# Kernel optimization log

Measured on AMD Instinct MI355X. Metric: run time of the kernel, lower is better.

## Reference

```python
import jax, jax.numpy as jnp
import numpy as np

V_IPC, N_ROLES, D = 50000, 16, 256
B, L = 2048, 64
F_BIB, H1, H2, D_OUT = 512, 1024, 1024, 512
N_EXP, N_CLS = 8, 10
LN_EPS = 1e-5


def setup_inputs() -> dict:
    key = jax.random.key(0)
    ks = jax.random.split(key, 24)
    s = 0.05
    ipc_emb = jax.random.normal(ks[0], (V_IPC, D), jnp.float32) * s
    ipc_emb = ipc_emb.at[0].set(0.0)  # padding_idx=0
    role_emb = jax.random.normal(ks[1], (N_ROLES, D), jnp.float32) * s
    role_emb = role_emb.at[0].set(0.0)
    inp = {
        "ipc_indices": jax.random.randint(ks[2], (B, L), 0, V_IPC),
        "role_indices": jax.random.randint(ks[3], (B, L), 0, N_ROLES),
        "bibliometric_features": jax.random.normal(ks[4], (B, F_BIB), jnp.float32),
        "ipc_padding_mask": jax.random.randint(ks[5], (B, L), 0, 2).astype(jnp.int32),
        "top_k": 2,
        "ipc_emb": ipc_emb,
        "role_emb": role_emb,
        "Wq": jax.random.normal(ks[6], (D, D), jnp.float32) * s,
        "bq": jnp.zeros((D,), jnp.float32),
        "Wk": jax.random.normal(ks[7], (D, D), jnp.float32) * s,
        "bk": jnp.zeros((D,), jnp.float32),
        "Wv": jax.random.normal(ks[8], (D, D), jnp.float32) * s,
        "bv": jnp.zeros((D,), jnp.float32),
        "global_context": jax.random.normal(ks[9], (D,), jnp.float32) * s,
        "ln_g": jnp.ones((D,), jnp.float32),
        "ln_b": jnp.zeros((D,), jnp.float32),
        "gate_W": jax.random.normal(ks[10], (D, N_EXP), jnp.float32) * s,
        "gate_b": jnp.zeros((N_EXP,), jnp.float32),
        "expert_biases": jnp.zeros((N_EXP,), jnp.float32),
        "W1": jax.random.normal(ks[11], (N_EXP, F_BIB, H1), jnp.float32) * s,
        "b1": jnp.zeros((N_EXP, H1), jnp.float32),
        "W2": jax.random.normal(ks[12], (N_EXP, H1, H2), jnp.float32) * s,
        "b2": jnp.zeros((N_EXP, H2), jnp.float32),
        "W3": jax.random.normal(ks[13], (N_EXP, H2, D_OUT), jnp.float32) * s,
        "b3": jnp.zeros((N_EXP, D_OUT), jnp.float32),
        "head_W": jax.random.normal(ks[14], (D_OUT, N_CLS), jnp.float32) * s,
        "head_b": jnp.zeros((N_CLS,), jnp.float32),
    }
    return inp


def reference(ipc_indices, role_indices, bibliometric_features, ipc_padding_mask, top_k,
              ipc_emb, role_emb, Wq, bq, Wk, bk, Wv, bv, global_context, ln_g, ln_b,
              gate_W, gate_b, expert_biases, W1, b1, W2, b2, W3, b3, head_W, head_b):
    # embeddings + role combine  -> [B, L, D]
    x = ipc_emb[ipc_indices] + role_emb[role_indices]
    # attention pooling with a global learned query (same query for every batch row)
    keys = x @ Wk + bk                                  # [B, L, D]
    values = x @ Wv + bv                                # [B, L, D]
    q = global_context @ Wq + bq                        # [D]
    scores = jnp.einsum('d,bld->bl', q, keys)           # [B, L]
    scores = jnp.where(ipc_padding_mask == 0, -1e9, scores)
    attn = jax.nn.softmax(scores, axis=-1)              # [B, L]
    pooled = jnp.einsum('bl,bld->bd', attn, values)     # [B, D]
    mu = pooled.mean(-1, keepdims=True)
    var = ((pooled - mu) ** 2).mean(-1, keepdims=True)
    router_in = (pooled - mu) / jnp.sqrt(var + LN_EPS) * ln_g + ln_b
    # router: select with biased scores, gate with unbiased scores
    affinity = router_in @ gate_W + gate_b              # [B, E]
    sel_scores = affinity + expert_biases
    _, idx = jax.lax.top_k(sel_scores, top_k)           # [B, K]
    gw = jax.nn.softmax(jnp.take_along_axis(affinity, idx, axis=-1), axis=-1)  # [B, K]
    # dense all-expert MLP (reference form of masked per-expert loop)
    h = jax.nn.relu(jnp.einsum('bi,eih->ebh', bibliometric_features, W1) + b1[:, None, :])
    h = jax.nn.relu(jnp.einsum('ebh,ehj->ebj', h, W2) + b2[:, None, :])
    eo = jnp.einsum('ebj,ejo->ebo', h, W3) + b3[:, None, :]  # [E, B, O]
    # gather each token's top-k expert outputs and combine
    bidx = jnp.arange(idx.shape[0])[:, None]            # [B, 1]
    sel_out = eo[idx, bidx]                             # [B, K, O]
    moe_out = jnp.einsum('bk,bko->bo', gw, sel_out)     # [B, O]
    logits = moe_out @ head_W + head_b                  # [B, n_classes]
    return logits, idx
```

## Files before the change

kernel.cpp:

```cpp
#include <hip/hip_runtime.h>
#include <hip/hip_bf16.h>
#include <math.h>


#define LN_EPS 1e-5f

typedef __bf16 bf16_t;
typedef __bf16 bf16x8 __attribute__((ext_vector_type(8)));
typedef float f32x4 __attribute__((ext_vector_type(4)));

struct f4x2 { float4 a, b; };
__device__ __forceinline__ f4x2 ldA8(const float* p) {
  f4x2 v; v.a = *(const float4*)p; v.b = *(const float4*)(p + 4); return v;
}
__device__ __forceinline__ bf16x8 cvt8(const f4x2& v) {
  bf16x8 o;
  o[0] = (bf16_t)v.a.x; o[1] = (bf16_t)v.a.y; o[2] = (bf16_t)v.a.z; o[3] = (bf16_t)v.a.w;
  o[4] = (bf16_t)v.b.x; o[5] = (bf16_t)v.b.y; o[6] = (bf16_t)v.b.z; o[7] = (bf16_t)v.b.w;
  return o;
}

__global__ __launch_bounds__(256)
void transpose_prep(const float* __restrict__ W1, const float* __restrict__ W2,
                    const float* __restrict__ W3, bf16_t* __restrict__ B1,
                    bf16_t* __restrict__ B2, bf16_t* __restrict__ B3,
                    const float* __restrict__ Wq, const float* __restrict__ bq,
                    const float* __restrict__ Wk, const float* __restrict__ bk,
                    const float* __restrict__ gc, float* __restrict__ kq_out) {
  __shared__ float tile[64][65];
  const int z = blockIdx.z;
  if (z == 24) {
    if (blockIdx.y >= 2) return;
    float* q = &tile[0][0];
    float* red = &tile[0][0] + 256;
    const int t = threadIdx.x, bi = blockIdx.y * 16 + blockIdx.x;
    float s = bq[t];
    for (int d = 0; d < 256; d++) s += gc[d] * Wq[d * 256 + t];
    q[t] = s;
    __syncthreads();
    const int rl = t >> 5, sl = t & 31;
    const int r = bi * 8 + rl;
    float p = 0.f;
#pragma unroll
    for (int i = 0; i < 8; i++) { const int d = sl + 32 * i; p += Wk[r * 256 + d] * q[d]; }
#pragma unroll
    for (int o = 16; o > 0; o >>= 1) p += __shfl_down(p, o, 32);
    if (sl == 0) kq_out[r] = p;
    if (bi == 0) {
      float z2 = q[t] * bk[t];
      const int lane = t & 63, wave = t >> 6;
#pragma unroll
      for (int o = 32; o > 0; o >>= 1) z2 += __shfl_down(z2, o);
      if (lane == 0) red[wave] = z2;
      __syncthreads();
      if (t == 0) kq_out[256] = red[0] + red[1] + red[2] + red[3];
    }
    return;
  }
  const float* W; bf16_t* Bft; int K, N, e;
  if (z < 8)       { W = W1; Bft = B1; K = 512;  N = 1024; e = z; }
  else if (z < 16) { W = W2; Bft = B2; K = 1024; N = 1024; e = z - 8; }
  else             { W = W3; Bft = B3; K = 1024; N = 512;  e = z - 16; }
  const int n0 = blockIdx.x * 64, k0 = blockIdx.y * 64;
  if (n0 >= N || k0 >= K) return;
  const float* Wp = W + (size_t)e * K * N;
  bf16_t* Bp = Bft + (size_t)e * N * K;
  const int tq = threadIdx.x & 15, th = threadIdx.x >> 4;
#pragma unroll
  for (int i = 0; i < 4; i++) {
    const int row = th + 16 * i;
    *(float4*)&tile[row][tq * 4] = *(const float4*)(Wp + (size_t)(k0 + row) * N + n0 + tq * 4);
  }
  __syncthreads();
  const int lane = threadIdx.x & 63, sub = threadIdx.x >> 6;
  const int nk = K >> 5;
#pragma unroll
  for (int it = 0; it < 2; it++) {
    const int fid = sub + it * 4;
    const int ntl = fid & 3, ktl = fid >> 2;
    const int n_l = ntl * 16 + (lane & 15);
    const int k_l = ktl * 32 + (lane >> 4) * 8;
    bf16x8 o;
#pragma unroll
    for (int j = 0; j < 8; j++) o[j] = (bf16_t)tile[k_l + j][n_l];
    const size_t idx = ((((size_t)(n0 >> 4) + ntl) * nk + (k0 >> 5) + ktl) * 64 + lane) * 8;
    *(bf16x8*)(Bp + idx) = o;
  }
}

__global__ __launch_bounds__(256)
void xbar_kernel(const int* __restrict__ ipc_idx, const int* __restrict__ role_idx,
                 const int* __restrict__ maskp,
                 const float* __restrict__ ipc_emb, const float* __restrict__ role_emb,
                 const float* __restrict__ kq_qbk, float* __restrict__ xbar_g) {
  const int b = blockIdx.x;
  __shared__ float scores_s[64];
  __shared__ float attn_s[64];
  __shared__ __align__(16) float part[4][256];
  const int t = threadIdx.x, wave = t >> 6, lane = t & 63;
  const float4 kq = *(const float4*)(kq_qbk + lane * 4);
  const float qbk = kq_qbk[256];
  const int rbase = b * 64 + wave * 16;
  float4 x[16];
  int mk[16];
#pragma unroll
  for (int i = 0; i < 16; i++) {
    mk[i] = maskp[rbase + i];
    if (mk[i] != 0) {
      const int ii = ipc_idx[rbase + i], ri = role_idx[rbase + i];
      const float4 xe = *(const float4*)(ipc_emb + (size_t)ii * 256 + lane * 4);
      const float4 re = *(const float4*)(role_emb + (size_t)ri * 256 + lane * 4);
      x[i] = make_float4(xe.x + re.x, xe.y + re.y, xe.z + re.z, xe.w + re.w);
    } else {
      x[i] = make_float4(0.f, 0.f, 0.f, 0.f);
    }
  }
#pragma unroll
  for (int i = 0; i < 16; i++) {
    float s;
    if (mk[i] != 0) {
      s = x[i].x * kq.x + x[i].y * kq.y + x[i].z * kq.z + x[i].w * kq.w;
#pragma unroll
      for (int o = 32; o > 0; o >>= 1) s += __shfl_xor(s, o);
      s += qbk;
    } else {
      s = -1e9f;
    }
    if (lane == 0) scores_s[wave * 16 + i] = s;
  }
  __syncthreads();
  if (wave == 0) {
    const float sv = scores_s[lane];
    float m = sv;
#pragma unroll
    for (int o = 32; o > 0; o >>= 1) m = fmaxf(m, __shfl_xor(m, o));
    const float ev = expf(sv - m);
    float sum = ev;
#pragma unroll
    for (int o = 32; o > 0; o >>= 1) sum += __shfl_xor(sum, o);
    attn_s[lane] = ev / sum;
  }
  __syncthreads();
  float p0 = 0.f, p1 = 0.f, p2 = 0.f, p3 = 0.f;
#pragma unroll
  for (int i = 0; i < 16; i++) {
    const float a = attn_s[wave * 16 + i];
    p0 += a * x[i].x; p1 += a * x[i].y; p2 += a * x[i].z; p3 += a * x[i].w;
  }
  *(float4*)&part[wave][lane * 4] = make_float4(p0, p1, p2, p3);
  __syncthreads();
  xbar_g[(size_t)b * 256 + t] = part[0][t] + part[1][t] + part[2][t] + part[3][t];
}

__global__ __launch_bounds__(256)
void pool_kernel(const float* __restrict__ xbar_g, const float* __restrict__ Wv,
                 const float* __restrict__ bvec,
                 const float* __restrict__ ln_g, const float* __restrict__ ln_b,
                 const float* __restrict__ gate_W, const float* __restrict__ gate_b,
                 const float* __restrict__ expert_biases,
                 float* __restrict__ out_idx_f, int* __restrict__ ws_idx,
                 float* __restrict__ ws_gw) {
  const int rb = blockIdx.x * 8;
  __shared__ __align__(16) float xs[8][256];
  __shared__ __align__(16) float pp[4][8][256];
  const int t = threadIdx.x, wave = t >> 6, lane = t & 63;
  for (int i = t; i < 512; i += 256)
    ((float4*)xs)[i] = ((const float4*)(xbar_g + (size_t)rb * 256))[i];
  __syncthreads();
  f32x4 acc[8];
#pragma unroll
  for (int r = 0; r < 8; r++) acc[r] = (f32x4){0.f, 0.f, 0.f, 0.f};
  const int dbase = wave * 64;
  for (int dd = 0; dd < 64; dd += 4) {
    float4 xr[8];
#pragma unroll
    for (int r = 0; r < 8; r++) xr[r] = *(const float4*)&xs[r][dbase + dd];
#pragma unroll
    for (int j = 0; j < 4; j++) {
      const float4 wv = *(const float4*)(Wv + (size_t)(dbase + dd + j) * 256 + lane * 4);
#pragma unroll
      for (int r = 0; r < 8; r++) {
        const float xv = (&xr[r].x)[j];
        acc[r][0] += xv * wv.x; acc[r][1] += xv * wv.y;
        acc[r][2] += xv * wv.z; acc[r][3] += xv * wv.w;
      }
    }
  }
#pragma unroll
  for (int r = 0; r < 8; r++) *(f32x4*)&pp[wave][r][lane * 4] = acc[r];
  __syncthreads();
  const float4 bvv = *(const float4*)(bvec + lane * 4);
  const float4 lg = *(const float4*)(ln_g + lane * 4);
  const float4 lb = *(const float4*)(ln_b + lane * 4);
#pragma unroll
  for (int rr = 0; rr < 2; rr++) {
    const int r = wave * 2 + rr;
    f32x4 v = *(const f32x4*)&pp[0][r][lane * 4];
#pragma unroll
    for (int w2 = 1; w2 < 4; w2++) {
      const f32x4 qv = *(const f32x4*)&pp[w2][r][lane * 4];
      v[0] += qv[0]; v[1] += qv[1]; v[2] += qv[2]; v[3] += qv[3];
    }
    v[0] += bvv.x; v[1] += bvv.y; v[2] += bvv.z; v[3] += bvv.w;
    float s1 = v[0] + v[1] + v[2] + v[3];
#pragma unroll
    for (int o = 32; o > 0; o >>= 1) s1 += __shfl_xor(s1, o);
    const float mu = s1 * (1.f / 256.f);
    const float4 df = make_float4(v[0] - mu, v[1] - mu, v[2] - mu, v[3] - mu);
    float s2 = df.x * df.x + df.y * df.y + df.z * df.z + df.w * df.w;
#pragma unroll
    for (int o = 32; o > 0; o >>= 1) s2 += __shfl_xor(s2, o);
    const float inv = 1.f / sqrtf(s2 * (1.f / 256.f) + LN_EPS);
    f32x4 rv;
    rv[0] = df.x * inv * lg.x + lb.x; rv[1] = df.y * inv * lg.y + lb.y;
    rv[2] = df.z * inv * lg.z + lb.z; rv[3] = df.w * inv * lg.w + lb.w;
    f32x4 pa = {0.f, 0.f, 0.f, 0.f}, pb = {0.f, 0.f, 0.f, 0.f};
#pragma unroll
    for (int k = 0; k < 4; k++) {
      const int d = lane * 4 + k;
      const f32x4 g0 = *(const f32x4*)(gate_W + d * 8);
      const f32x4 g1 = *(const f32x4*)(gate_W + d * 8 + 4);
      pa += rv[k] * g0;
      pb += rv[k] * g1;
    }
#pragma unroll
    for (int o = 32; o > 0; o >>= 1) {
      pa[0] += __shfl_down(pa[0], o); pa[1] += __shfl_down(pa[1], o);
      pa[2] += __shfl_down(pa[2], o); pa[3] += __shfl_down(pa[3], o);
      pb[0] += __shfl_down(pb[0], o); pb[1] += __shfl_down(pb[1], o);
      pb[2] += __shfl_down(pb[2], o); pb[3] += __shfl_down(pb[3], o);
    }
    if (lane == 0) {
      float aff[8];
#pragma unroll
      for (int j = 0; j < 4; j++) { aff[j] = pa[j] + gate_b[j]; aff[4 + j] = pb[j] + gate_b[4 + j]; }
      float b0 = -1e30f; int i0 = 0;
#pragma unroll
      for (int j = 0; j < 8; j++) {
        const float s = aff[j] + expert_biases[j];
        if (s > b0) { b0 = s; i0 = j; }
      }
      float b1v = -1e30f; int i1 = 0;
#pragma unroll
      for (int j = 0; j < 8; j++) {
        const float s = aff[j] + expert_biases[j];
        if (j != i0 && s > b1v) { b1v = s; i1 = j; }
      }
      const float a0 = aff[i0], a1 = aff[i1];
      const float m = fmaxf(a0, a1);
      const float e0 = expf(a0 - m), e1 = expf(a1 - m);
      const float invs = 1.f / (e0 + e1);
      const int bg = rb + r;
      ws_idx[bg * 2] = i0; ws_idx[bg * 2 + 1] = i1;
      ws_gw[bg * 2] = e0 * invs; ws_gw[bg * 2 + 1] = e1 * invs;
      out_idx_f[bg * 2] = (float)i0; out_idx_f[bg * 2 + 1] = (float)i1;
    }
  }
}

__global__ __launch_bounds__(256)
void pack_kernel(const int* __restrict__ ws_idx, int* __restrict__ list_token,
                 int* __restrict__ a_of, int* __restrict__ offsets_g) {
  __shared__ int cnt[8]; __shared__ int off[9]; __shared__ int fill[8];
  const int t = threadIdx.x;
  if (t < 8) cnt[t] = 0;
  __syncthreads();
  for (int a = t; a < 4096; a += 256) atomicAdd(&cnt[ws_idx[a]], 1);
  __syncthreads();
  if (t == 0) {
    off[0] = 0;
    for (int e = 0; e < 8; e++) off[e + 1] = off[e] + ((cnt[e] + 63) & ~63);
  }
  __syncthreads();
  if (t < 8) fill[t] = off[t];
  if (t < 9) offsets_g[t] = off[t];
  for (int a = t; a < 4608; a += 256) list_token[a] = 0;
  __syncthreads();
  for (int a = t; a < 4096; a += 256) {
    const int e = ws_idx[a];
    const int pos = atomicAdd(&fill[e], 1);
    list_token[pos] = a >> 1;
    a_of[a] = pos;
  }
}

template <int NT, bool RELU>
__global__ __launch_bounds__(256)
void expert_gemm_g1(const float* __restrict__ bib, const int* __restrict__ list_token,
                    const bf16_t* __restrict__ Bft, const float* __restrict__ bias,
                    bf16_t* __restrict__ C, const int* __restrict__ offsets) {
  constexpr int K = 512, nk = K / 32;
  const int e = blockIdx.z;
  const int seg_hi = offsets[e + 1];
  const int blk_row = offsets[e] + blockIdx.y * 128;
  if (blk_row >= seg_hi) return;
  const int wave = threadIdx.x >> 6, lane = threadIdx.x & 63;
  const int row0 = blk_row + wave * 32;
  if (row0 >= seg_hi) return;
  const int n0 = blockIdx.x * 64;
  const int tok0 = list_token[row0 + (lane & 15)];
  const int tok1 = list_token[row0 + 16 + (lane & 15)];
  const float* Ap0 = bib + (size_t)tok0 * 512 + (lane >> 4) * 8;
  const float* Ap1 = bib + (size_t)tok1 * 512 + (lane >> 4) * 8;
  const bf16_t* Bp = Bft + (size_t)e * NT * K + ((size_t)(n0 >> 4) * nk * 512 + lane * 8);
  f32x4 acc[2][4];
#pragma unroll
  for (int i = 0; i < 2; i++)
#pragma unroll
    for (int j = 0; j < 4; j++) acc[i][j] = (f32x4){0.f, 0.f, 0.f, 0.f};
  f4x2 aS[2][2]; bf16x8 bX[2][4];
  aS[0][0] = ldA8(Ap0); aS[0][1] = ldA8(Ap1);
#pragma unroll
  for (int ni = 0; ni < 4; ni++) bX[0][ni] = *(const bf16x8*)(Bp + (size_t)ni * nk * 512);
#pragma unroll
  for (int kt = 0; kt < nk; kt++) {
    const int cur = kt & 1, nxt = cur ^ 1;
    if (kt + 1 < nk) {
      aS[nxt][0] = ldA8(Ap0 + (kt + 1) * 32);
      aS[nxt][1] = ldA8(Ap1 + (kt + 1) * 32);
#pragma unroll
      for (int ni = 0; ni < 4; ni++)
        bX[nxt][ni] = *(const bf16x8*)(Bp + ((size_t)ni * nk + kt + 1) * 512);
    }
    const bf16x8 a0 = cvt8(aS[cur][0]), a1 = cvt8(aS[cur][1]);
#pragma unroll
    for (int ni = 0; ni < 4; ni++) {
      acc[0][ni] = __builtin_amdgcn_mfma_f32_16x16x32_bf16(a0, bX[cur][ni], acc[0][ni], 0, 0, 0);
      acc[1][ni] = __builtin_amdgcn_mfma_f32_16x16x32_bf16(a1, bX[cur][ni], acc[1][ni], 0, 0, 0);
    }
  }
  const int fr = lane & 15, q = lane >> 4;
#pragma unroll
  for (int ni = 0; ni < 4; ni++) {
    const int col = n0 + ni * 16 + fr;
    const float bv = bias[e * NT + col];
#pragma unroll
    for (int mi = 0; mi < 2; mi++) {
#pragma unroll
      for (int r = 0; r < 4; r++) {
        const int row = row0 + mi * 16 + q * 4 + r;
        float v = acc[mi][ni][r] + bv;
        if (RELU) v = fmaxf(v, 0.f);
        C[(size_t)row * NT + col] = (bf16_t)v;
      }
    }
  }
}

template <int K, int NT, bool RELU, typename OUT_T>
__global__ __launch_bounds__(256)
void expert_gemm_ft(const bf16_t* __restrict__ A, const bf16_t* __restrict__ Bft,
                    const float* __restrict__ bias, OUT_T* __restrict__ C,
                    const int* __restrict__ offsets) {
  constexpr int nk = K / 32;
  const int e = blockIdx.z;
  const int seg_hi = offsets[e + 1];
  const int blk_row = offsets[e] + blockIdx.y * 128;
  if (blk_row >= seg_hi) return;
  const int wave = threadIdx.x >> 6, lane = threadIdx.x & 63;
  const int row0 = blk_row + wave * 32;
  if (row0 >= seg_hi) return;
  const int n0 = blockIdx.x * 64;
  const bf16_t* Ap = A + (size_t)(row0 + (lane & 15)) * K + ((lane >> 4) * 8);
  const bf16_t* Bp = Bft + (size_t)e * NT * K + ((size_t)(n0 >> 4) * nk * 512 + lane * 8);
  f32x4 acc[2][4];
#pragma unroll
  for (int i = 0; i < 2; i++)
#pragma unroll
    for (int j = 0; j < 4; j++) acc[i][j] = (f32x4){0.f, 0.f, 0.f, 0.f};
  bf16x8 aX[2][2], bX[2][4];
#pragma unroll
  for (int mi = 0; mi < 2; mi++) aX[0][mi] = *(const bf16x8*)(Ap + mi * 16 * K);
#pragma unroll
  for (int ni = 0; ni < 4; ni++) bX[0][ni] = *(const bf16x8*)(Bp + (size_t)ni * nk * 512);
#pragma unroll
  for (int kt = 0; kt < nk; kt++) {
    const int cur = kt & 1, nxt = cur ^ 1;
    if (kt + 1 < nk) {
#pragma unroll
      for (int mi = 0; mi < 2; mi++)
        aX[nxt][mi] = *(const bf16x8*)(Ap + mi * 16 * K + (kt + 1) * 32);
#pragma unroll
      for (int ni = 0; ni < 4; ni++)
        bX[nxt][ni] = *(const bf16x8*)(Bp + ((size_t)ni * nk + kt + 1) * 512);
    }
#pragma unroll
    for (int mi = 0; mi < 2; mi++)
#pragma unroll
      for (int ni = 0; ni < 4; ni++)
        acc[mi][ni] = __builtin_amdgcn_mfma_f32_16x16x32_bf16(aX[cur][mi], bX[cur][ni], acc[mi][ni], 0, 0, 0);
  }
  const int fr = lane & 15, q = lane >> 4;
#pragma unroll
  for (int ni = 0; ni < 4; ni++) {
    const int col = n0 + ni * 16 + fr;
    const float bv = bias[e * NT + col];
#pragma unroll
    for (int mi = 0; mi < 2; mi++) {
#pragma unroll
      for (int r = 0; r < 4; r++) {
        const int row = row0 + mi * 16 + q * 4 + r;
        float v = acc[mi][ni][r] + bv;
        if (RELU) v = fmaxf(v, 0.f);
        C[(size_t)row * NT + col] = (OUT_T)v;
      }
    }
  }
}

__global__ __launch_bounds__(256)
void head_kernel(const float* __restrict__ O, const int* __restrict__ a_of,
                 const float* __restrict__ ws_gw, const float* __restrict__ head_W,
                 const float* __restrict__ head_b, float* __restrict__ out) {
  const int b = blockIdx.x, t = threadIdx.x;
  __shared__ float m[512];
  const int a0 = a_of[b * 2], a1 = a_of[b * 2 + 1];
  const float g0 = ws_gw[b * 2], g1 = ws_gw[b * 2 + 1];
  for (int d = t; d < 512; d += 256)
    m[d] = g0 * O[(size_t)a0 * 512 + d] + g1 * O[(size_t)a1 * 512 + d];
  __syncthreads();
  if (t < 160) {
    const int c = t >> 4, ch = t & 15;
    float p = 0.f;
#pragma unroll
    for (int i = 0; i < 32; i++) {
      const int d = i * 16 + ch;
      p += m[d] * head_W[d * 10 + c];
    }
#pragma unroll
    for (int o = 8; o > 0; o >>= 1) p += __shfl_down(p, o, 16);
    if (ch == 0) out[b * 10 + c] = p + head_b[c];
  }
}

extern "C" void kernel_launch(void* const* d_in, const int* in_sizes, int n_in,
                              void* d_out, int out_size, void* d_ws, size_t ws_size,
                              hipStream_t stream) {
  const int* ipc_idx = (const int*)d_in[0];
  const int* role_idx = (const int*)d_in[1];
  const float* bib = (const float*)d_in[2];
  const int* maskp = (const int*)d_in[3];
  const float* ipc_emb = (const float*)d_in[5];
  const float* role_emb = (const float*)d_in[6];
  const float* Wq = (const float*)d_in[7];
  const float* bq = (const float*)d_in[8];
  const float* Wk = (const float*)d_in[9];
  const float* bk = (const float*)d_in[10];
  const float* Wv = (const float*)d_in[11];
  const float* bv = (const float*)d_in[12];
  const float* gc = (const float*)d_in[13];
  const float* ln_g = (const float*)d_in[14];
  const float* ln_b = (const float*)d_in[15];
  const float* gate_W = (const float*)d_in[16];
  const float* gate_b = (const float*)d_in[17];
  const float* exp_b = (const float*)d_in[18];
  const float* W1 = (const float*)d_in[19];
  const float* b1 = (const float*)d_in[20];
  const float* W2 = (const float*)d_in[21];
  const float* b2 = (const float*)d_in[22];
  const float* W3 = (const float*)d_in[23];
  const float* b3 = (const float*)d_in[24];
  const float* head_W = (const float*)d_in[25];
  const float* head_b = (const float*)d_in[26];

  char* ws = (char*)d_ws;
  size_t off = 0;
  auto alloc = [&](size_t bytes) -> char* {
    char* p = ws + off;
    off += (bytes + 255) & ~(size_t)255;
    return p;
  };
  float* kq_qbk = (float*)alloc(257 * 4);
  float* xbar_g = (float*)alloc((size_t)2048 * 256 * 4);
  int* ws_idx = (int*)alloc(4096 * 4);
  float* ws_gw = (float*)alloc(4096 * 4);
  int* list_tok = (int*)alloc(4608 * 4);
  int* a_of = (int*)alloc(4096 * 4);
  int* offs = (int*)alloc(9 * 4);
  bf16_t* W1t = (bf16_t*)alloc((size_t)8 * 1024 * 512 * 2);
  bf16_t* W2t = (bf16_t*)alloc((size_t)8 * 1024 * 1024 * 2);
  bf16_t* W3t = (bf16_t*)alloc((size_t)8 * 512 * 1024 * 2);
  bf16_t* H1c = (bf16_t*)alloc((size_t)4608 * 1024 * 2);
  bf16_t* H2c = (bf16_t*)alloc((size_t)4608 * 1024 * 2);
  float* Oc = (float*)alloc((size_t)4608 * 512 * 4);
  (void)in_sizes; (void)n_in; (void)out_size; (void)ws_size;

  float* out_logits = (float*)d_out;
  float* out_idx = (float*)d_out + 20480;

  transpose_prep<<<dim3(16, 16, 25), 256, 0, stream>>>(W1, W2, W3, W1t, W2t, W3t,
                                                       Wq, bq, Wk, bk, gc, kq_qbk);
  xbar_kernel<<<2048, 256, 0, stream>>>(ipc_idx, role_idx, maskp, ipc_emb, role_emb,
                                        kq_qbk, xbar_g);
  pool_kernel<<<256, 256, 0, stream>>>(xbar_g, Wv, bv, ln_g, ln_b, gate_W, gate_b,
                                       exp_b, out_idx, ws_idx, ws_gw);
  pack_kernel<<<1, 256, 0, stream>>>(ws_idx, list_tok, a_of, offs);
  expert_gemm_g1<1024, true><<<dim3(16, 36, 8), 256, 0, stream>>>(bib, list_tok, W1t, b1, H1c, offs);
  expert_gemm_ft<1024, 1024, true, bf16_t><<<dim3(16, 36, 8), 256, 0, stream>>>(H1c, W2t, b2, H2c, offs);
  expert_gemm_ft<1024, 512, false, float><<<dim3(8, 36, 8), 256, 0, stream>>>(H2c, W3t, b3, Oc, offs);
  head_kernel<<<2048, 256, 0, stream>>>(Oc, a_of, ws_gw, head_W, head_b, out_logits);
}
```

Before: 370.0 us.

## Fuse attention pooling with weight transpose and defer score reductions via LDS

The kq projection moves into its own small kernel. The attention-pooling blocks are merged with the expert-weight transpose/bf16 conversion into one launch, so the latency-bound gather work can overlap the bandwidth-bound transpose. Inside the xbar path, per-row shuffle reductions become partial dot products stored in LDS and reduced together. Embeddings are re-gathered in the second pass instead of being held in registers, which lowers register pressure at the cost of twice the gather traffic. Masked rows now load row 0 unconditionally and use vectorised int4 index loads.

```diff
diff --git a/kernel.cpp b/kernel.cpp
--- a/kernel.cpp
+++ b/kernel.cpp
@@ -21,58 +21,142 @@
 }
 
 __global__ __launch_bounds__(256)
-void transpose_prep(const float* __restrict__ W1, const float* __restrict__ W2,
+void prep_kq_kernel(const float* __restrict__ Wq, const float* __restrict__ bq,
+                    const float* __restrict__ Wk, const float* __restrict__ bk,
+                    const float* __restrict__ gc, float* __restrict__ kq_out) {
+  __shared__ float q[256];
+  __shared__ float red[4];
+  const int t = threadIdx.x, bi = blockIdx.x;
+  float s = bq[t];
+  for (int d = 0; d < 256; d++) s += gc[d] * Wq[d * 256 + t];
+  q[t] = s;
+  __syncthreads();
+  const int rl = t >> 5, sl = t & 31;
+  const int r = bi * 8 + rl;
+  float p = 0.f;
+#pragma unroll
+  for (int i = 0; i < 8; i++) { const int d = sl + 32 * i; p += Wk[r * 256 + d] * q[d]; }
+#pragma unroll
+  for (int o = 16; o > 0; o >>= 1) p += __shfl_down(p, o, 32);
+  if (sl == 0) kq_out[r] = p;
+  if (bi == 0) {
+    float z2 = q[t] * bk[t];
+    const int lane = t & 63, wave = t >> 6;
+#pragma unroll
+    for (int o = 32; o > 0; o >>= 1) z2 += __shfl_down(z2, o);
+    if (lane == 0) red[wave] = z2;
+    __syncthreads();
+    if (t == 0) kq_out[256] = red[0] + red[1] + red[2] + red[3];
+  }
+}
+
+__global__ __launch_bounds__(256)
+void xbar_transpose(const float* __restrict__ W1, const float* __restrict__ W2,
                     const float* __restrict__ W3, bf16_t* __restrict__ B1,
                     bf16_t* __restrict__ B2, bf16_t* __restrict__ B3,
-                    const float* __restrict__ Wq, const float* __restrict__ bq,
-                    const float* __restrict__ Wk, const float* __restrict__ bk,
-                    const float* __restrict__ gc, float* __restrict__ kq_out) {
-  __shared__ float tile[64][65];
-  const int z = blockIdx.z;
-  if (z == 24) {
-    if (blockIdx.y >= 2) return;
-    float* q = &tile[0][0];
-    float* red = &tile[0][0] + 256;
-    const int t = threadIdx.x, bi = blockIdx.y * 16 + blockIdx.x;
-    float s = bq[t];
-    for (int d = 0; d < 256; d++) s += gc[d] * Wq[d * 256 + t];
-    q[t] = s;
+                    const int* __restrict__ ipc_idx, const int* __restrict__ role_idx,
+                    const int* __restrict__ maskp,
+                    const float* __restrict__ ipc_emb, const float* __restrict__ role_emb,
+                    const float* __restrict__ kq_qbk, float* __restrict__ xbar_g) {
+  __shared__ __align__(16) float smem[4480];
+  const int bid = blockIdx.x;
+  const int t = threadIdx.x, lane = t & 63;
+
+  if (bid < 2048) {
+    const int b = bid, wave = t >> 6;
+    float* sred = smem;
+    float* scores_s = smem + 4352;
+    float* attn_s = smem + 4416;
+    const float4 kq = *(const float4*)(kq_qbk + lane * 4);
+    const float qbk = kq_qbk[256];
+    const int rbase = b * 64 + wave * 16;
+    int4 m4[4], i4[4], r4[4];
+#pragma unroll
+    for (int j = 0; j < 4; j++) {
+      m4[j] = *(const int4*)(maskp + rbase + j * 4);
+      i4[j] = *(const int4*)(ipc_idx + rbase + j * 4);
+      r4[j] = *(const int4*)(role_idx + rbase + j * 4);
+    }
+#pragma unroll
+    for (int i = 0; i < 16; i++) {
+      const int mki = (&m4[i / 4].x)[i % 4];
+      const int ii = mki ? (&i4[i / 4].x)[i % 4] : 0;
+      const int ri = mki ? (&r4[i / 4].x)[i % 4] : 0;
+      const float4 xe = *(const float4*)(ipc_emb + (size_t)ii * 256 + lane * 4);
+      const float4 re = *(const float4*)(role_emb + (size_t)ri * 256 + lane * 4);
+      sred[(wave * 64 + lane) * 17 + i] =
+          (xe.x + re.x) * kq.x + (xe.y + re.y) * kq.y +
+          (xe.z + re.z) * kq.z + (xe.w + re.w) * kq.w;
+    }
     __syncthreads();
-    const int rl = t >> 5, sl = t & 31;
-    const int r = bi * 8 + rl;
-    float p = 0.f;
-#pragma unroll
-    for (int i = 0; i < 8; i++) { const int d = sl + 32 * i; p += Wk[r * 256 + d] * q[d]; }
-#pragma unroll
-    for (int o = 16; o > 0; o >>= 1) p += __shfl_down(p, o, 32);
-    if (sl == 0) kq_out[r] = p;
-    if (bi == 0) {
-      float z2 = q[t] * bk[t];
-      const int lane = t & 63, wave = t >> 6;
-#pragma unroll
-      for (int o = 32; o > 0; o >>= 1) z2 += __shfl_down(z2, o);
-      if (lane == 0) red[wave] = z2;
-      __syncthreads();
-      if (t == 0) kq_out[256] = red[0] + red[1] + red[2] + red[3];
-    }
+    {
+      const int i_r = lane & 15, g = lane >> 4;
+      float s = 0.f;
+#pragma unroll
+      for (int j = 0; j < 16; j++) s += sred[(wave * 64 + g * 16 + j) * 17 + i_r];
+      s += __shfl_xor(s, 16);
+      s += __shfl_xor(s, 32);
+      const int mval = maskp[rbase + i_r];
+      if (lane < 16) scores_s[wave * 16 + lane] = mval ? (s + qbk) : -1e9f;
+    }
+    __syncthreads();
+    if (wave == 0) {
+      const float sv = scores_s[lane];
+      float m = sv;
+#pragma unroll
+      for (int o = 32; o > 0; o >>= 1) m = fmaxf(m, __shfl_xor(m, o));
+      const float ev = expf(sv - m);
+      float sum = ev;
+#pragma unroll
+      for (int o = 32; o > 0; o >>= 1) sum += __shfl_xor(sum, o);
+      attn_s[lane] = ev / sum;
+    }
+    __syncthreads();
+    float p0 = 0.f, p1 = 0.f, p2 = 0.f, p3 = 0.f;
+#pragma unroll
+    for (int i = 0; i < 16; i++) {
+      const int mki = (&m4[i / 4].x)[i % 4];
+      const int ii = mki ? (&i4[i / 4].x)[i % 4] : 0;
+      const int ri = mki ? (&r4[i / 4].x)[i % 4] : 0;
+      const float a = attn_s[wave * 16 + i];
+      const float4 xe = *(const float4*)(ipc_emb + (size_t)ii * 256 + lane * 4);
+      const float4 re = *(const float4*)(role_emb + (size_t)ri * 256 + lane * 4);
+      p0 += a * (xe.x + re.x); p1 += a * (xe.y + re.y);
+      p2 += a * (xe.z + re.z); p3 += a * (xe.w + re.w);
+    }
+    __syncthreads();
+    *(float4*)&smem[wave * 256 + lane * 4] = make_float4(p0, p1, p2, p3);
+    __syncthreads();
+    xbar_g[(size_t)b * 256 + t] = smem[t] + smem[256 + t] + smem[512 + t] + smem[768 + t];
     return;
   }
-  const float* W; bf16_t* Bft; int K, N, e;
-  if (z < 8)       { W = W1; Bft = B1; K = 512;  N = 1024; e = z; }
-  else if (z < 16) { W = W2; Bft = B2; K = 1024; N = 1024; e = z - 8; }
-  else             { W = W3; Bft = B3; K = 1024; N = 512;  e = z - 16; }
-  const int n0 = blockIdx.x * 64, k0 = blockIdx.y * 64;
-  if (n0 >= N || k0 >= K) return;
+
+  const int bid2 = bid - 2048;
+  const float* W; bf16_t* Bft; int K, N, e, n0, k0;
+  if (bid2 < 1024) {
+    W = W1; Bft = B1; K = 512; N = 1024;
+    e = bid2 >> 7; const int r = bid2 & 127;
+    n0 = (r & 15) * 64; k0 = (r >> 4) * 64;
+  } else if (bid2 < 3072) {
+    W = W2; Bft = B2; K = 1024; N = 1024;
+    const int q = bid2 - 1024; e = q >> 8; const int r = q & 255;
+    n0 = (r & 15) * 64; k0 = (r >> 4) * 64;
+  } else {
+    W = W3; Bft = B3; K = 1024; N = 512;
+    const int q = bid2 - 3072; e = q >> 7; const int r = q & 127;
+    n0 = (r & 7) * 64; k0 = (r >> 3) * 64;
+  }
+  float (*tile)[65] = (float(*)[65])smem;
   const float* Wp = W + (size_t)e * K * N;
   bf16_t* Bp = Bft + (size_t)e * N * K;
-  const int tq = threadIdx.x & 15, th = threadIdx.x >> 4;
+  const int tq = t & 15, th = t >> 4;
 #pragma unroll
   for (int i = 0; i < 4; i++) {
     const int row = th + 16 * i;
     *(float4*)&tile[row][tq * 4] = *(const float4*)(Wp + (size_t)(k0 + row) * N + n0 + tq * 4);
   }
   __syncthreads();
-  const int lane = threadIdx.x & 63, sub = threadIdx.x >> 6;
+  const int sub = t >> 6;
   const int nk = K >> 5;
 #pragma unroll
   for (int it = 0; it < 2; it++) {
@@ -86,70 +170,6 @@
     const size_t idx = ((((size_t)(n0 >> 4) + ntl) * nk + (k0 >> 5) + ktl) * 64 + lane) * 8;
     *(bf16x8*)(Bp + idx) = o;
   }
-}
-
-__global__ __launch_bounds__(256)
-void xbar_kernel(const int* __restrict__ ipc_idx, const int* __restrict__ role_idx,
-                 const int* __restrict__ maskp,
-                 const float* __restrict__ ipc_emb, const float* __restrict__ role_emb,
-                 const float* __restrict__ kq_qbk, float* __restrict__ xbar_g) {
-  const int b = blockIdx.x;
-  __shared__ float scores_s[64];
-  __shared__ float attn_s[64];
-  __shared__ __align__(16) float part[4][256];
-  const int t = threadIdx.x, wave = t >> 6, lane = t & 63;
-  const float4 kq = *(const float4*)(kq_qbk + lane * 4);
-  const float qbk = kq_qbk[256];
-  const int rbase = b * 64 + wave * 16;
-  float4 x[16];
-  int mk[16];
-#pragma unroll
-  for (int i = 0; i < 16; i++) {
-    mk[i] = maskp[rbase + i];
-    if (mk[i] != 0) {
-      const int ii = ipc_idx[rbase + i], ri = role_idx[rbase + i];
-      const float4 xe = *(const float4*)(ipc_emb + (size_t)ii * 256 + lane * 4);
-      const float4 re = *(const float4*)(role_emb + (size_t)ri * 256 + lane * 4);
-      x[i] = make_float4(xe.x + re.x, xe.y + re.y, xe.z + re.z, xe.w + re.w);
-    } else {
-      x[i] = make_float4(0.f, 0.f, 0.f, 0.f);
-    }
-  }
-#pragma unroll
-  for (int i = 0; i < 16; i++) {
-    float s;
-    if (mk[i] != 0) {
-      s = x[i].x * kq.x + x[i].y * kq.y + x[i].z * kq.z + x[i].w * kq.w;
-#pragma unroll
-      for (int o = 32; o > 0; o >>= 1) s += __shfl_xor(s, o);
-      s += qbk;
-    } else {
-      s = -1e9f;
-    }
-    if (lane == 0) scores_s[wave * 16 + i] = s;
-  }
-  __syncthreads();
-  if (wave == 0) {
-    const float sv = scores_s[lane];
-    float m = sv;
-#pragma unroll
-    for (int o = 32; o > 0; o >>= 1) m = fmaxf(m, __shfl_xor(m, o));
-    const float ev = expf(sv - m);
-    float sum = ev;
-#pragma unroll
-    for (int o = 32; o > 0; o >>= 1) sum += __shfl_xor(sum, o);
-    attn_s[lane] = ev / sum;
-  }
-  __syncthreads();
-  float p0 = 0.f, p1 = 0.f, p2 = 0.f, p3 = 0.f;
-#pragma unroll
-  for (int i = 0; i < 16; i++) {
-    const float a = attn_s[wave * 16 + i];
-    p0 += a * x[i].x; p1 += a * x[i].y; p2 += a * x[i].z; p3 += a * x[i].w;
-  }
-  *(float4*)&part[wave][lane * 4] = make_float4(p0, p1, p2, p3);
-  __syncthreads();
-  xbar_g[(size_t)b * 256 + t] = part[0][t] + part[1][t] + part[2][t] + part[3][t];
 }
 
 __global__ __launch_bounds__(256)
@@ -488,10 +508,10 @@
   float* out_logits = (float*)d_out;
   float* out_idx = (float*)d_out + 20480;
 
-  transpose_prep<<<dim3(16, 16, 25), 256, 0, stream>>>(W1, W2, W3, W1t, W2t, W3t,
-                                                       Wq, bq, Wk, bk, gc, kq_qbk);
-  xbar_kernel<<<2048, 256, 0, stream>>>(ipc_idx, role_idx, maskp, ipc_emb, role_emb,
-                                        kq_qbk, xbar_g);
+  prep_kq_kernel<<<32, 256, 0, stream>>>(Wq, bq, Wk, bk, gc, kq_qbk);
+  xbar_transpose<<<6144, 256, 0, stream>>>(W1, W2, W3, W1t, W2t, W3t,
+                                           ipc_idx, role_idx, maskp,
+                                           ipc_emb, role_emb, kq_qbk, xbar_g);
   pool_kernel<<<256, 256, 0, stream>>>(xbar_g, Wv, bv, ln_g, ln_b, gate_W, gate_b,
                                        exp_b, out_idx, ws_idx, ws_gw);
   pack_kernel<<<1, 256, 0, stream>>>(ws_idx, list_tok, a_of, offs);
```

New measurement: 356.3 us. 1.04x faster.
